# Performance work log

Hardware: AMD Instinct MI355X
Metric: run time of the kernel (lower is better)

Reference implementation:

```python
import jax, jax.numpy as jnp
import numpy as np

NUM_HEADS = 4
EPS = 1e-12  # torch F.normalize eps


def _l2norm(t):
    # normalize along last axis, matching torch.nn.functional.normalize
    n = jnp.sqrt(jnp.sum(t * t, axis=-1, keepdims=True))
    return t / jnp.maximum(n, EPS)


def setup_inputs() -> dict:
    key = jax.random.key(0)
    k1, k2 = jax.random.split(key)
    B, N, C = 4, 8192, 768
    x = jax.random.normal(k1, (B, N, C), dtype=jnp.float32)
    W_qkvv = jax.random.normal(k2, (3 * C, C), dtype=jnp.float32) * (C ** -0.5)
    temperature = jnp.ones((NUM_HEADS, 1, 1), dtype=jnp.float32)
    return {"x": x, "W_qkvv": W_qkvv, "temperature": temperature}


def reference(x, W_qkvv, temperature):
    B, N, C = x.shape
    H = NUM_HEADS
    D = C // H
    # qkvv projection: [B,N,3C] -> [3,B,H,N,D]
    qkvv = (x @ W_qkvv.T).reshape(B, N, 3, H, D).transpose(2, 0, 3, 1, 4)
    q, k, v = qkvv[0], qkvv[1], qkvv[2]        # each [B,H,N,D]
    q = jnp.swapaxes(q, -2, -1)                # [B,H,D,N]
    k = jnp.swapaxes(k, -2, -1)                # [B,H,D,N]
    v = jnp.swapaxes(v, -2, -1)                # [B,H,D,N]
    q = _l2norm(q)
    k = _l2norm(k)
    # channel attention scores: [B,H,D,D], temperature broadcast per head
    attn = jnp.einsum('bhdn,bhen->bhde', q, k) * temperature[None]
    attn = jax.nn.softmax(attn, axis=-1)
    # dropout is identity in eval mode
    x_CA = jnp.einsum('bhde,bhen->bhdn', attn, v)   # [B,H,D,N]
    out = x_CA.transpose(0, 3, 1, 2).reshape(B, N, C)
    return out
```

## Files before the change

kernel.cpp:

```cpp
#include <hip/hip_runtime.h>
#include <hip/hip_bf16.h>
#include <cstddef>
#include <cstdint>

#define B_   4
#define N_   8192
#define C_   768
#define H_   4
#define D_   192
#define CQ_  2304
#define M_   32768

typedef __attribute__((ext_vector_type(8))) short short8_t;
typedef __attribute__((ext_vector_type(4))) float f32x4;

typedef const __attribute__((address_space(1))) uint gq_uint;
typedef __attribute__((address_space(3))) uint lds_uint;

__device__ inline ushort f2bf(float f){
  uint u = __float_as_uint(f);
  u += 0x7FFFu + ((u >> 16) & 1u);
  return (ushort)(u >> 16);
}
__device__ inline float bf2f(ushort u){ return __uint_as_float(((uint)u) << 16); }

__global__ __launch_bounds__(256) void cvt_bf16(const float* __restrict__ src,
                                                ushort* __restrict__ dst, int n4){
  int i = blockIdx.x * 256 + threadIdx.x;
  if (i < n4){
    float4 v = ((const float4*)src)[i];
    ushort4 o;
    o.x = f2bf(v.x); o.y = f2bf(v.y); o.z = f2bf(v.z); o.w = f2bf(v.w);
    ((ushort4*)dst)[i] = o;
  }
}

__global__ __launch_bounds__(512, 2) void gemm_qkvv(const ushort* __restrict__ A,
                                                    const ushort* __restrict__ W,
                                                    ushort* __restrict__ Cq,
                                                    float* __restrict__ norm2){
  extern __shared__ ushort lds[];
  const int t = threadIdx.x;
  const int bid = blockIdx.x;
  const int wg  = (bid & 7) * 144 + (bid >> 3);
  const int by = wg / 9, bx = wg % 9;
  const int m0 = by * 256, n0 = bx * 256;
  const int wid = t >> 6, lane = t & 63;
  const int wm = wid >> 2, wn = wid & 3;
  const int lr = lane & 15, lg = lane >> 4;
  const int srow  = lane >> 3;
  const int sslot = (lane & 7) ^ srow;

  f32x4 acc[8][4];
  #pragma unroll
  for (int i = 0; i < 8; ++i)
    #pragma unroll
    for (int j = 0; j < 4; ++j)
      acc[i][j] = (f32x4){0.f, 0.f, 0.f, 0.f};

  #define STAGE_HALF(GPTR, G0, KT, LBASE, HALF)                                 \
    do {                                                                        \
      _Pragma("unroll")                                                         \
      for (int rnd_ = 0; rnd_ < 2; ++rnd_){                                     \
        const int row_ = (HALF) * 128 + rnd_ * 64 + wid * 8;                    \
        __builtin_amdgcn_global_load_lds(                                       \
            (gq_uint*)(const void*)((GPTR) + (size_t)((G0) + row_ + srow) * 768 \
                                    + (KT) * 64 + sslot * 8),                   \
            (lds_uint*)(void*)((LBASE) + row_ * 64), 16, 0, 0);                 \
      }                                                                         \
    } while (0)

  #define RD_A(DST, MH)                                                         \
    _Pragma("unroll") for (int kk = 0; kk < 2; ++kk){                           \
      const int sl = ((kk * 4 + lg) ^ (lr & 7)) * 8;                            \
      _Pragma("unroll") for (int fm = 0; fm < 4; ++fm)                          \
        DST[kk][fm] = *(const short8_t*)(bA + ((MH)*128 + wm*64 + fm*16 + lr)*64 + sl); }

  #define RD_B(DST, NH)                                                         \
    _Pragma("unroll") for (int kk = 0; kk < 2; ++kk){                           \
      const int sl = ((kk * 4 + lg) ^ (lr & 7)) * 8;                            \
      _Pragma("unroll") for (int fl = 0; fl < 2; ++fl)                          \
        DST[kk][fl] = *(const short8_t*)(bB + ((NH)*128 + wn*32 + fl*16 + lr)*64 + sl); }

  #define MM(AR, BR, IO, JO)                                                    \
    __builtin_amdgcn_s_setprio(1);                                              \
    _Pragma("unroll") for (int kk = 0; kk < 2; ++kk)                            \
    _Pragma("unroll") for (int fm = 0; fm < 4; ++fm)                            \
    _Pragma("unroll") for (int fl = 0; fl < 2; ++fl)                            \
      acc[(IO)+fm][(JO)+fl] = __builtin_amdgcn_mfma_f32_16x16x32_bf16(          \
          AR[kk][fm], BR[kk][fl], acc[(IO)+fm][(JO)+fl], 0, 0, 0);              \
    __builtin_amdgcn_s_setprio(0);

  #define WAITP(N)                                                              \
    asm volatile("s_waitcnt vmcnt(" #N ")" ::: "memory");                       \
    __builtin_amdgcn_s_barrier();                                               \
    asm volatile("s_waitcnt lgkmcnt(0)" ::: "memory");                          \
    __builtin_amdgcn_sched_barrier(0);

  STAGE_HALF(A, m0, 0, lds,         0);
  STAGE_HALF(A, m0, 0, lds,         1);
  STAGE_HALF(W, n0, 0, lds + 16384, 0);
  STAGE_HALF(W, n0, 0, lds + 16384, 1);
  asm volatile("s_waitcnt vmcnt(0)" ::: "memory");
  __builtin_amdgcn_s_barrier();
  __builtin_amdgcn_sched_barrier(0);

  short8_t a0[2][4], a1[2][4], bf0[2][2], bf1[2][2];

  #pragma unroll 2
  for (int kt = 0; kt < 11; ++kt){
    const ushort* bA = lds + (kt & 1) * 32768;
    const ushort* bB = bA + 16384;
    ushort* nA = lds + ((kt + 1) & 1) * 32768;
    ushort* nB = nA + 16384;
    RD_A(a0, 0); RD_B(bf0, 0);
    STAGE_HALF(A, m0, kt + 1, nA, 0);
    WAITP(4);
    MM(a0, bf0, 0, 0);
    RD_A(a1, 1);
    STAGE_HALF(W, n0, kt + 1, nB, 0);
    WAITP(4);
    MM(a1, bf0, 4, 0);
    RD_B(bf1, 1);
    STAGE_HALF(A, m0, kt + 1, nA, 1);
    WAITP(4);
    MM(a1, bf1, 4, 2);
    STAGE_HALF(W, n0, kt + 1, nB, 1);
    WAITP(4);
    MM(a0, bf1, 0, 2);
  }
  {
    const ushort* bA = lds + 32768;
    const ushort* bB = bA + 16384;
    RD_A(a0, 0); RD_B(bf0, 0);
    WAITP(2);
    MM(a0, bf0, 0, 0);
    RD_A(a1, 1);
    WAITP(0);
    MM(a1, bf0, 4, 0);
    RD_B(bf1, 1);
    asm volatile("s_waitcnt lgkmcnt(0)" ::: "memory");
    __builtin_amdgcn_sched_barrier(0);
    MM(a1, bf1, 4, 2);
    MM(a0, bf1, 0, 2);
  }
  #undef STAGE_HALF
  #undef RD_A
  #undef RD_B
  #undef MM
  #undef WAITP

  #pragma unroll
  for (int i = 0; i < 8; ++i)
    #pragma unroll
    for (int j = 0; j < 4; ++j)
      #pragma unroll
      for (int r = 0; r < 4; ++r){
        int m = m0 + (i >> 2) * 128 + wm * 64 + (i & 3) * 16 + lg * 4 + r;
        int c = n0 + (j >> 1) * 128 + wn * 32 + (j & 1) * 16 + lr;
        Cq[(size_t)m * CQ_ + c] = f2bf(acc[i][j][r]);
      }

  if (bx < 6){
    const int b = m0 >> 13;
    #pragma unroll
    for (int j = 0; j < 4; ++j){
      float s = 0.f;
      #pragma unroll
      for (int i = 0; i < 8; ++i)
        #pragma unroll
        for (int r = 0; r < 4; ++r)
          s = fmaf(acc[i][j][r], acc[i][j][r], s);
      s += __shfl_xor(s, 16);
      s += __shfl_xor(s, 32);
      if (lg == 0)
        atomicAdd(&norm2[b * 1536 + n0 + (j >> 1) * 128 + wn * 32 + (j & 1) * 16 + lr], s);
    }
  }
}

__global__ __launch_bounds__(512) void gram_mfma(const ushort* __restrict__ Qk,
                                                 float* __restrict__ Sp){
  const int kc = blockIdx.x;
  const int bh = blockIdx.y;
  const int b = bh >> 2, h = bh & 3;
  __shared__ __align__(16) ushort qs[32][194];
  __shared__ __align__(16) ushort ks[32][194];
  const int t = threadIdx.x;
  const int wid = t >> 6, lane = t & 63;
  const int wd = wid >> 2, we = wid & 3;
  const int lr = lane & 15, lg = lane >> 4;

  f32x4 acc[6][3];
  #pragma unroll
  for (int i = 0; i < 6; ++i)
    #pragma unroll
    for (int j = 0; j < 3; ++j)
      acc[i][j] = (f32x4){0.f, 0.f, 0.f, 0.f};

  const uint* qb = (const uint*)Qk + ((size_t)b * N_ * CQ_) / 2 + h * 96;
  const uint* kb = qb + 384;

  for (int it = 0; it < 16; ++it){
    const int n0 = kc * 512 + it * 32;
    __syncthreads();
    #pragma unroll
    for (int u = 0; u < 6; ++u){
      int g = u * 512 + t;
      int row = g / 96, c = g % 96;
      ((uint*)qs[row])[c] = qb[(size_t)(n0 + row) * 1152 + c];
      ((uint*)ks[row])[c] = kb[(size_t)(n0 + row) * 1152 + c];
    }
    __syncthreads();
    union { uint u[4]; short8_t v; } af[6], bf[3];
    #pragma unroll
    for (int i = 0; i < 6; ++i){
      int d = wd * 96 + i * 16 + lr;
      #pragma unroll
      for (int p = 0; p < 4; ++p)
        af[i].u[p] = (uint)qs[lg*8 + 2*p][d] | ((uint)qs[lg*8 + 2*p + 1][d] << 16);
    }
    #pragma unroll
    for (int j = 0; j < 3; ++j){
      int e = we * 48 + j * 16 + lr;
      #pragma unroll
      for (int p = 0; p < 4; ++p)
        bf[j].u[p] = (uint)ks[lg*8 + 2*p][e] | ((uint)ks[lg*8 + 2*p + 1][e] << 16);
    }
    #pragma unroll
    for (int i = 0; i < 6; ++i)
      #pragma unroll
      for (int j = 0; j < 3; ++j)
        acc[i][j] = __builtin_amdgcn_mfma_f32_16x16x32_bf16(af[i].v, bf[j].v, acc[i][j], 0, 0, 0);
  }
  float* base = Sp + (size_t)(kc * 16 + bh) * 192 * 192;
  #pragma unroll
  for (int i = 0; i < 6; ++i)
    #pragma unroll
    for (int j = 0; j < 3; ++j)
      #pragma unroll
      for (int r = 0; r < 4; ++r){
        int d = wd * 96 + i * 16 + lg * 4 + r;
        int e = we * 48 + j * 16 + lr;
        base[(size_t)d * 192 + e] = acc[i][j][r];
      }
}

__global__ __launch_bounds__(256) void softmax_k(const float* __restrict__ Sp,
                                                 const float* __restrict__ norm2,
                                                 const float* __restrict__ temp,
                                                 ushort* __restrict__ attn){
  const int wid  = blockIdx.x * 4 + (threadIdx.x >> 6);
  const int lane = threadIdx.x & 63;
  const int bh = wid / 192, d = wid % 192;
  const int b = bh >> 2, h = bh & 3;
  const float nq = sqrtf(norm2[b*1536 + h*192 + d]);
  const float sc = temp[h] / fmaxf(nq, 1e-12f);
  const float* Sr = Sp + ((size_t)bh * 192 + d) * 192;
  float l[3];
  #pragma unroll
  for (int u = 0; u < 3; ++u){
    int e = lane + u * 64;
    float s = 0.f;
    #pragma unroll
    for (int kc = 0; kc < 16; ++kc)
      s += Sr[(size_t)kc * (16*192*192) + e];
    float nk = sqrtf(norm2[b*1536 + 768 + h*192 + e]);
    l[u] = s * sc / fmaxf(nk, 1e-12f);
  }
  float m = fmaxf(l[0], fmaxf(l[1], l[2]));
  #pragma unroll
  for (int off = 32; off; off >>= 1) m = fmaxf(m, __shfl_xor(m, off));
  float p[3], s = 0.f;
  #pragma unroll
  for (int u = 0; u < 3; ++u){ p[u] = expf(l[u] - m); s += p[u]; }
  #pragma unroll
  for (int off = 32; off; off >>= 1) s += __shfl_xor(s, off);
  float inv = 1.f / s;
  ushort* ar = attn + ((size_t)bh * 192 + d) * 192;
  #pragma unroll
  for (int u = 0; u < 3; ++u) ar[lane + u*64] = f2bf(p[u] * inv);
}

__global__ __launch_bounds__(256) void out_gemm(const ushort* __restrict__ Q,
                                                const ushort* __restrict__ attn,
                                                float* __restrict__ out){
  const int bh = blockIdx.y;
  const int b = bh >> 2, h = bh & 3;
  const int n0 = blockIdx.x * 128;
  const int t = threadIdx.x, w = t >> 6, lane = t & 63;
  const int wn = w & 1, wd = w >> 1;
  const int lr = lane & 15, lg = lane >> 4;
  f32x4 acc[4][6];
  #pragma unroll
  for (int i = 0; i < 4; ++i)
    #pragma unroll
    for (int j = 0; j < 6; ++j)
      acc[i][j] = (f32x4){0.f, 0.f, 0.f, 0.f};

  const ushort* Vbase = Q + 1536 + h * 192;
  const ushort* Abase = attn + (size_t)bh * 192 * 192;

  #pragma unroll
  for (int kk = 0; kk < 6; ++kk){
    const int e = kk * 32 + lg * 8;
    short8_t av[4], bv[6];
    #pragma unroll
    for (int f = 0; f < 4; ++f){
      int n = n0 + wn*64 + f*16 + lr;
      av[f] = *(const short8_t*)(Vbase + (size_t)(b*N_ + n) * CQ_ + e);
    }
    #pragma unroll
    for (int f = 0; f < 6; ++f){
      int d = wd*96 + f*16 + lr;
      bv[f] = *(const short8_t*)(Abase + d * 192 + e);
    }
    #pragma unroll
    for (int i = 0; i < 4; ++i)
      #pragma unroll
      for (int j = 0; j < 6; ++j)
        acc[i][j] = __builtin_amdgcn_mfma_f32_16x16x32_bf16(av[i], bv[j], acc[i][j], 0, 0, 0);
  }
  #pragma unroll
  for (int i = 0; i < 4; ++i)
    #pragma unroll
    for (int j = 0; j < 6; ++j)
      #pragma unroll
      for (int r = 0; r < 4; ++r){
        int n = n0 + wn*64 + i*16 + lg*4 + r;
        int c = h*192 + wd*96 + j*16 + lr;
        out[(size_t)(b*N_ + n) * 768 + c] = acc[i][j][r];
      }
}

extern "C" void kernel_launch(void* const* d_in, const int* in_sizes, int n_in,
                              void* d_out, int out_size, void* d_ws, size_t ws_size,
                              hipStream_t stream){
  const float* x    = (const float*)d_in[0];
  const float* Wq   = (const float*)d_in[1];
  const float* temp = (const float*)d_in[2];
  float* out = (float*)d_out;
  char* ws = (char*)d_ws;

  ushort* xb    = (ushort*)(ws + 0);
  float*  S_part= (float*)(ws + 0);
  ushort* attn  = (ushort*)(ws + 37748736);
  ushort* Wb    = (ushort*)(ws + 50331648);
  ushort* qkvv  = (ushort*)(ws + 53870592);
  float*  norm2 = (float*)(ws + 204865536);

  static_assert(sizeof(ushort) == 2, "");
  hipFuncSetAttribute((const void*)gemm_qkvv,
                      hipFuncAttributeMaxDynamicSharedMemorySize, 131072);

  hipMemsetAsync(norm2, 0, 24576, stream);

  cvt_bf16<<<6291456/256, 256, 0, stream>>>(x,  xb, 6291456);
  cvt_bf16<<<442368/256,  256, 0, stream>>>(Wq, Wb, 442368);

  gemm_qkvv<<<1152, 512, 131072, stream>>>(xb, Wb, qkvv, norm2);

  gram_mfma<<<dim3(16, 16), 512, 0, stream>>>(qkvv, S_part);
  softmax_k<<<768, 256, 0, stream>>>(S_part, norm2, temp, attn);
  out_gemm<<<dim3(64, 16), 256, 0, stream>>>(qkvv, attn, out);
}
```

Baseline: 246.1 us.

## Split GEMM LDS waits from barriers and double-buffer pre-packed gram tiles

In the projection GEMM, the combined vmcnt/barrier/lgkmcnt wait is split so the next LDS fragment reads are issued before the MFMA block and only partially drained. This lets LDS reads overlap with matrix math. The gram kernel now uses register-prefetched global loads and a double-buffered LDS tile that stores row pairs already packed into 32-bit words. This replaces per-element 16-bit gathers with single 32-bit reads and removes one barrier per iteration. The trade-offs are higher register use and more reliance on exact waitcnt accounting.

```diff
diff --git a/kernel.cpp b/kernel.cpp
--- a/kernel.cpp
+++ b/kernel.cpp
@@ -91,10 +91,13 @@
           AR[kk][fm], BR[kk][fl], acc[(IO)+fm][(JO)+fl], 0, 0, 0);              \
     __builtin_amdgcn_s_setprio(0);
 
-  #define WAITP(N)                                                              \
+  #define VWAIT(N)                                                              \
     asm volatile("s_waitcnt vmcnt(" #N ")" ::: "memory");                       \
     __builtin_amdgcn_s_barrier();                                               \
-    asm volatile("s_waitcnt lgkmcnt(0)" ::: "memory");                          \
+    __builtin_amdgcn_sched_barrier(0);
+
+  #define LWAIT(N)                                                              \
+    asm volatile("s_waitcnt lgkmcnt(" #N ")" ::: "memory");                     \
     __builtin_amdgcn_sched_barrier(0);
 
   STAGE_HALF(A, m0, 0, lds,         0);
@@ -115,32 +118,38 @@
     ushort* nB = nA + 16384;
     RD_A(a0, 0); RD_B(bf0, 0);
     STAGE_HALF(A, m0, kt + 1, nA, 0);
-    WAITP(4);
+    VWAIT(4);
+    RD_A(a1, 1);
+    LWAIT(8);
     MM(a0, bf0, 0, 0);
-    RD_A(a1, 1);
     STAGE_HALF(W, n0, kt + 1, nB, 0);
-    WAITP(4);
+    VWAIT(4);
+    RD_B(bf1, 1);
+    LWAIT(4);
     MM(a1, bf0, 4, 0);
-    RD_B(bf1, 1);
     STAGE_HALF(A, m0, kt + 1, nA, 1);
-    WAITP(4);
+    VWAIT(4);
+    LWAIT(0);
     MM(a1, bf1, 4, 2);
     STAGE_HALF(W, n0, kt + 1, nB, 1);
-    WAITP(4);
+    VWAIT(4);
     MM(a0, bf1, 0, 2);
   }
   {
     const ushort* bA = lds + 32768;
     const ushort* bB = bA + 16384;
     RD_A(a0, 0); RD_B(bf0, 0);
-    WAITP(2);
+    VWAIT(2);
+    RD_A(a1, 1);
+    LWAIT(8);
     MM(a0, bf0, 0, 0);
-    RD_A(a1, 1);
-    WAITP(0);
+    asm volatile("s_waitcnt vmcnt(0)" ::: "memory");
+    __builtin_amdgcn_s_barrier();
+    __builtin_amdgcn_sched_barrier(0);
+    RD_B(bf1, 1);
+    LWAIT(4);
     MM(a1, bf0, 4, 0);
-    RD_B(bf1, 1);
-    asm volatile("s_waitcnt lgkmcnt(0)" ::: "memory");
-    __builtin_amdgcn_sched_barrier(0);
+    LWAIT(0);
     MM(a1, bf1, 4, 2);
     MM(a0, bf1, 0, 2);
   }
@@ -148,7 +157,8 @@
   #undef RD_A
   #undef RD_B
   #undef MM
-  #undef WAITP
+  #undef VWAIT
+  #undef LWAIT
 
   #pragma unroll
   for (int i = 0; i < 8; ++i)
@@ -184,8 +194,7 @@
   const int kc = blockIdx.x;
   const int bh = blockIdx.y;
   const int b = bh >> 2, h = bh & 3;
-  __shared__ __align__(16) ushort qs[32][194];
-  __shared__ __align__(16) ushort ks[32][194];
+  __shared__ __align__(16) uint pk[2][2][3232];
   const int t = threadIdx.x;
   const int wid = t >> 6, lane = t & 63;
   const int wd = wid >> 2, we = wid & 3;
@@ -198,41 +207,59 @@
     for (int j = 0; j < 3; ++j)
       acc[i][j] = (f32x4){0.f, 0.f, 0.f, 0.f};
 
-  const uint* qb = (const uint*)Qk + ((size_t)b * N_ * CQ_) / 2 + h * 96;
-  const uint* kb = qb + 384;
+  const uint* gq = (const uint*)Qk + (size_t)b * N_ * 1152;
+
+  uint r0[6], r1[6];
+  #define GLOAD(IT)                                                             \
+    _Pragma("unroll") for (int u = 0; u < 6; ++u){                              \
+      int id = u*512 + t, mat = id/1536, rem = id - mat*1536;                   \
+      int np = rem/96, c = rem - np*96;                                         \
+      const uint* p = gq + (size_t)(kc*512 + (IT)*32 + 2*np)*1152               \
+                         + (mat ? 384 + h*96 : h*96) + c;                       \
+      r0[u] = p[0]; r1[u] = p[1152];                                            \
+    }
+  #define LWRITE(BUF)                                                           \
+    _Pragma("unroll") for (int u = 0; u < 6; ++u){                              \
+      int id = u*512 + t, mat = id/1536, rem = id - mat*1536;                   \
+      int np = rem/96, c = rem - np*96;                                         \
+      uint o0 = (r0[u] & 0xFFFFu) | (r1[u] << 16);                              \
+      uint o1 = (r0[u] >> 16) | (r1[u] & 0xFFFF0000u);                          \
+      *(uint2*)&pk[BUF][mat][np*202 + 2*c] = (uint2){o0, o1};                   \
+    }
+
+  GLOAD(0);
+  LWRITE(0);
+  __syncthreads();
 
   for (int it = 0; it < 16; ++it){
-    const int n0 = kc * 512 + it * 32;
-    __syncthreads();
-    #pragma unroll
-    for (int u = 0; u < 6; ++u){
-      int g = u * 512 + t;
-      int row = g / 96, c = g % 96;
-      ((uint*)qs[row])[c] = qb[(size_t)(n0 + row) * 1152 + c];
-      ((uint*)ks[row])[c] = kb[(size_t)(n0 + row) * 1152 + c];
-    }
-    __syncthreads();
+    const int cur = it & 1;
+    if (it < 15) GLOAD(it + 1);
     union { uint u[4]; short8_t v; } af[6], bf[3];
     #pragma unroll
     for (int i = 0; i < 6; ++i){
       int d = wd * 96 + i * 16 + lr;
       #pragma unroll
       for (int p = 0; p < 4; ++p)
-        af[i].u[p] = (uint)qs[lg*8 + 2*p][d] | ((uint)qs[lg*8 + 2*p + 1][d] << 16);
+        af[i].u[p] = pk[cur][0][(lg*4 + p)*202 + d];
     }
     #pragma unroll
     for (int j = 0; j < 3; ++j){
       int e = we * 48 + j * 16 + lr;
       #pragma unroll
       for (int p = 0; p < 4; ++p)
-        bf[j].u[p] = (uint)ks[lg*8 + 2*p][e] | ((uint)ks[lg*8 + 2*p + 1][e] << 16);
+        bf[j].u[p] = pk[cur][1][(lg*4 + p)*202 + e];
     }
     #pragma unroll
     for (int i = 0; i < 6; ++i)
       #pragma unroll
       for (int j = 0; j < 3; ++j)
         acc[i][j] = __builtin_amdgcn_mfma_f32_16x16x32_bf16(af[i].v, bf[j].v, acc[i][j], 0, 0, 0);
-  }
+    if (it < 15) LWRITE(cur ^ 1);
+    __syncthreads();
+  }
+  #undef GLOAD
+  #undef LWRITE
+
   float* base = Sp + (size_t)(kc * 16 + bh) * 192 * 192;
   #pragma unroll
   for (int i = 0; i < 6; ++i)
```

Result: slower. 302.1 us (+22.7%).
